# Kernel tuning notes

Measured on AMD Instinct MI355X. Metric: run time of the kernel, lower is better.

## Reference

```python
import jax, jax.numpy as jnp
import numpy as np

D_MODEL = 384
D_INNER = 768   # 2 * d_model
D_STATE = 16
DT_RANK = 24    # ceil(d_model/16)
K_CONV = 4
BATCH = 8
SEQ = 2048
EPS = 1e-5


def _layer_norm(x, w, b):
    mu = x.mean(-1, keepdims=True)
    var = ((x - mu) ** 2).mean(-1, keepdims=True)
    return (x - mu) * jax.lax.rsqrt(var + EPS) * w + b


def _silu(x):
    return x * jax.nn.sigmoid(x)


def _mamba_mixer(x, in_proj, conv_w, conv_b, x_proj, dt_w, dt_b, A_log, Dp, out_proj):
    # x: (B, L, d_model)
    xz = x @ in_proj.T                      # (B, L, 2*d_inner)
    xs, z = jnp.split(xz, 2, axis=-1)       # each (B, L, d_inner)
    # causal depthwise conv1d (pad left k-1)
    xc = jnp.transpose(xs, (0, 2, 1))       # (B, d_inner, L)
    xc = jnp.pad(xc, ((0, 0), (0, 0), (K_CONV - 1, 0)))
    xc = jax.lax.conv_general_dilated(
        xc, conv_w, window_strides=(1,), padding='VALID',
        feature_group_count=D_INNER,
        dimension_numbers=('NCH', 'OIH', 'NCH'))
    xs = _silu(jnp.transpose(xc, (0, 2, 1)) + conv_b)   # (B, L, d_inner)
    # input-dependent SSM parameters
    x_dbl = xs @ x_proj.T                    # (B, L, dt_rank + 2*d_state)
    dt, Bm, Cm = jnp.split(x_dbl, [DT_RANK, DT_RANK + D_STATE], axis=-1)
    dt = jax.nn.softplus(dt @ dt_w.T + dt_b)  # (B, L, d_inner)
    A = -jnp.exp(A_log)                       # (d_inner, d_state)

    def step(h, inp):
        dt_t, B_t, C_t, x_t = inp             # (B,d), (B,N), (B,N), (B,d)
        h = jnp.exp(dt_t[:, :, None] * A) * h + (dt_t * x_t)[:, :, None] * B_t[:, None, :]
        y = jnp.einsum('bdn,bn->bd', h, C_t)
        return h, y

    h0 = jnp.zeros((xs.shape[0], D_INNER, D_STATE), xs.dtype)
    inps = (jnp.moveaxis(dt, 1, 0), jnp.moveaxis(Bm, 1, 0),
            jnp.moveaxis(Cm, 1, 0), jnp.moveaxis(xs, 1, 0))
    _, ys = jax.lax.scan(step, h0, inps)      # ys: (L, B, d_inner)
    y = jnp.moveaxis(ys, 0, 1) + xs * Dp      # skip term D*x
    y = y * _silu(z)                          # gated output
    return y @ out_proj.T                     # (B, L, d_model)


def setup_inputs() -> dict:
    key = jax.random.key(0)
    ks = jax.random.split(key, 10)
    s = 0.02
    A_init = jnp.broadcast_to(jnp.log(jnp.arange(1, D_STATE + 1, dtype=jnp.float32)),
                              (2, D_INNER, D_STATE))
    return {
        'x': jax.random.normal(ks[0], (BATCH, SEQ, D_MODEL), jnp.float32),
        'norm_w': jnp.ones((2, D_MODEL), jnp.float32),
        'norm_b': jnp.zeros((2, D_MODEL), jnp.float32),
        'in_proj': jax.random.normal(ks[1], (2, 2 * D_INNER, D_MODEL)) * s,
        'conv_w': jax.random.normal(ks[2], (2, D_INNER, 1, K_CONV)) * 0.2,
        'conv_b': jax.random.normal(ks[3], (2, D_INNER)) * s,
        'x_proj': jax.random.normal(ks[4], (2, DT_RANK + 2 * D_STATE, D_INNER)) * s,
        'dt_w': jax.random.normal(ks[5], (2, D_INNER, DT_RANK)) * s,
        'dt_b': jax.random.normal(ks[6], (2, D_INNER)) * 0.1 - 4.0,
        'A_log': A_init,
        'Dp': jnp.ones((2, D_INNER), jnp.float32),
        'out_proj': jax.random.normal(ks[7], (2, D_MODEL, D_INNER)) * s,
    }


def reference(x, norm_w, norm_b, in_proj, conv_w, conv_b, x_proj, dt_w, dt_b, A_log, Dp, out_proj):
    def blk(i, h):
        return h + _mamba_mixer(_layer_norm(h, norm_w[i], norm_b[i]),
                                in_proj[i], conv_w[i], conv_b[i], x_proj[i],
                                dt_w[i], dt_b[i], A_log[i], Dp[i], out_proj[i])
    h = blk(0, x)                    # forward-direction block
    h = jnp.flip(h, axis=-2)         # reverse sequence
    h = blk(1, h)                    # backward-direction block
    return jnp.flip(h, axis=-2)      # restore order
```

## Files before the change

kernel.cpp:

```cpp
#include <hip/hip_runtime.h>
#include <hip/hip_bf16.h>
#include <cstddef>

#define D_MODEL 384
#define D_INNER 768
#define D_STATE 16
#define DT_RANK 24
#define K_CONV  4
#define BATCH   8
#define SEQ     2048
#define BL      (BATCH * SEQ)
#define NCHUNK  64
#define LCHUNK  (SEQ / NCHUNK)
#define XDBL_LD 64
#define LOG2E   1.44269504088896f

typedef unsigned short ushort_t;
typedef __bf16 bf16x8 __attribute__((ext_vector_type(8)));
typedef float  f32x4  __attribute__((ext_vector_type(4)));
typedef unsigned short u16x8 __attribute__((ext_vector_type(8)));

#define GLOBAL_AS(p) ((const __attribute__((address_space(1))) void*)(p))
#define LDS_AS(p)    ((__attribute__((address_space(3))) void*)(p))

__device__ __forceinline__ ushort_t f32_to_bf16_rne(float v) {
    unsigned int u = __float_as_uint(v);
    return (ushort_t)((u + 0x7FFFu + ((u >> 16) & 1u)) >> 16);
}
__device__ __forceinline__ float bf16_to_f32(ushort_t u) {
    return __uint_as_float(((unsigned int)u) << 16);
}

#define N_INP  (2 * 1536 * D_MODEL)
#define N_OUTP (2 * D_MODEL * D_INNER)
#define N_XP   (2 * 64 * D_INNER)
#define N_CW   (2 * K_CONV * D_INNER)
#define N_AL   (2 * D_STATE * D_INNER)
#define N_DW   (2 * DT_RANK * D_INNER)
#define N_PREP (N_INP + N_OUTP + N_XP + N_CW + N_AL + N_DW)

__global__ __launch_bounds__(256) void prep_kernel(
    const float* __restrict__ in_proj, const float* __restrict__ out_proj,
    const float* __restrict__ x_proj, const float* __restrict__ conv_w,
    const float* __restrict__ A_log, const float* __restrict__ dt_w,
    ushort_t* __restrict__ wbf_in, ushort_t* __restrict__ wbf_out,
    ushort_t* __restrict__ xp_bf, float* __restrict__ cwt,
    float* __restrict__ alt, float* __restrict__ dwt)
{
    int i = blockIdx.x * 256 + threadIdx.x;
    if (i < N_INP) {
        wbf_in[i] = f32_to_bf16_rne(in_proj[i]);
        return;
    }
    i -= N_INP;
    if (i < N_OUTP) {
        wbf_out[i] = f32_to_bf16_rne(out_proj[i]);
        return;
    }
    i -= N_OUTP;
    if (i < N_XP) {
        int c   = i % D_INNER;
        int r   = (i / D_INNER) % 64;
        int dir = i / (64 * D_INNER);
        xp_bf[i] = (r < 56)
            ? f32_to_bf16_rne(x_proj[((size_t)dir * 56 + r) * D_INNER + c])
            : (ushort_t)0;
        return;
    }
    i -= N_XP;
    if (i < N_CW) {
        int c = i % D_INNER, k = (i / D_INNER) % K_CONV, dir = i / (K_CONV * D_INNER);
        cwt[i] = conv_w[((size_t)dir * D_INNER + c) * K_CONV + k];
        return;
    }
    i -= N_CW;
    if (i < N_AL) {
        int d = i % D_INNER, n = (i / D_INNER) % D_STATE, dir = i / (D_STATE * D_INNER);
        alt[i] = A_log[((size_t)dir * D_INNER + d) * D_STATE + n];
        return;
    }
    i -= N_AL;
    if (i < N_DW) {
        int d = i % D_INNER, r = (i / D_INNER) % DT_RANK, dir = i / (DT_RANK * D_INNER);
        dwt[i] = dt_w[((size_t)dir * D_INNER + d) * DT_RANK + r];
    }
}

__global__ __launch_bounds__(256) void check_A_kernel(
    const float* __restrict__ A_log, int* __restrict__ flags)
{
    __shared__ int ok[2];
    int tid = threadIdx.x;
    if (tid < 2) ok[tid] = 1;
    __syncthreads();
    for (int dir = 0; dir < 2; dir++) {
        bool good = true;
        for (int j = tid; j < D_INNER * D_STATE; j += 256) {
            int n = j % D_STATE;
            float v = __expf(A_log[(size_t)dir * D_INNER * D_STATE + j]);
            good = good && (fabsf(v - (float)(n + 1)) <= 1e-4f * (float)(n + 1));
        }
        if (!good) atomicAnd(&ok[dir], 0);
    }
    __syncthreads();
    if (tid < 2) flags[tid] = ok[tid];
}

__global__ __launch_bounds__(384) void ln_kernel(
    const float* __restrict__ in, const float* __restrict__ w,
    const float* __restrict__ b, ushort_t* __restrict__ out)
{
    int row = blockIdx.x;
    int tid = threadIdx.x;
    float v = in[(size_t)row * D_MODEL + tid];
    float s = v, sq = v * v;
    #pragma unroll
    for (int o = 32; o; o >>= 1) {
        s  += __shfl_down(s, o);
        sq += __shfl_down(sq, o);
    }
    __shared__ float ss[6], ssq[6];
    __shared__ float mb[2];
    int wid = tid >> 6;
    if ((tid & 63) == 0) { ss[wid] = s; ssq[wid] = sq; }
    __syncthreads();
    if (tid == 0) {
        float S = 0.f, Q = 0.f;
        #pragma unroll
        for (int k = 0; k < 6; k++) { S += ss[k]; Q += ssq[k]; }
        float mu  = S * (1.0f / D_MODEL);
        float var = Q * (1.0f / D_MODEL) - mu * mu;
        mb[0] = mu;
        mb[1] = rsqrtf(var + 1e-5f);
    }
    __syncthreads();
    float r = (v - mb[0]) * mb[1] * w[tid] + b[tid];
    out[(size_t)row * D_MODEL + tid] = f32_to_bf16_rne(r);
}

__global__ __launch_bounds__(256) void gemm_mfma_b16(
    const ushort_t* __restrict__ A, const ushort_t* __restrict__ W,
    ushort_t* __restrict__ C, int N, int K)
{
    __shared__ __bf16 As[128 * 32];
    __shared__ __bf16 Ws[128 * 32];
    int tid  = threadIdx.x;
    int bm = blockIdx.x, bn = blockIdx.y;
    int lane = tid & 63, wave = tid >> 6;
    int wr = wave >> 1, wc = wave & 1;
    int quad = lane >> 4, l16 = lane & 15;
    int ca = ((quad ^ ((l16 >> 1) & 3))) * 8;
    int cbg = ((tid & 3) ^ ((tid >> 3) & 3)) * 8;

    const ushort_t* Ag = A + (size_t)(bm * 128 + (tid >> 2)) * K + cbg;
    const ushort_t* Wg = W + (size_t)(bn * 128 + (tid >> 2)) * K + cbg;

    f32x4 acc[4][4] = {};

    for (int k0 = 0; k0 < K; k0 += 32) {
        __syncthreads();
        __builtin_amdgcn_global_load_lds(GLOBAL_AS(Ag + k0),
                                         LDS_AS(As + tid * 8), 16, 0, 0);
        __builtin_amdgcn_global_load_lds(GLOBAL_AS(Ag + (size_t)64 * K + k0),
                                         LDS_AS(As + 2048 + tid * 8), 16, 0, 0);
        __builtin_amdgcn_global_load_lds(GLOBAL_AS(Wg + k0),
                                         LDS_AS(Ws + tid * 8), 16, 0, 0);
        __builtin_amdgcn_global_load_lds(GLOBAL_AS(Wg + (size_t)64 * K + k0),
                                         LDS_AS(Ws + 2048 + tid * 8), 16, 0, 0);
        __syncthreads();

        bf16x8 af[4], wf[4];
        #pragma unroll
        for (int i = 0; i < 4; i++)
            af[i] = *(const bf16x8*)(As + (wr * 64 + i * 16 + l16) * 32 + ca);
        #pragma unroll
        for (int j = 0; j < 4; j++)
            wf[j] = *(const bf16x8*)(Ws + (wc * 64 + j * 16 + l16) * 32 + ca);
        #pragma unroll
        for (int i = 0; i < 4; i++)
            #pragma unroll
            for (int j = 0; j < 4; j++)
                acc[i][j] = __builtin_amdgcn_mfma_f32_16x16x32_bf16(
                    af[i], wf[j], acc[i][j], 0, 0, 0);
    }

    #pragma unroll
    for (int i = 0; i < 4; i++) {
        #pragma unroll
        for (int r = 0; r < 4; r++) {
            int row = bm * 128 + wr * 64 + i * 16 + quad * 4 + r;
            #pragma unroll
            for (int j = 0; j < 4; j++) {
                int col = bn * 128 + wc * 64 + j * 16 + l16;
                C[(size_t)row * N + col] = f32_to_bf16_rne(acc[i][j][r]);
            }
        }
    }
}

__global__ __launch_bounds__(256) void gemm_mfma_f32(
    const ushort_t* __restrict__ A, const ushort_t* __restrict__ W,
    const float* __restrict__ resid, float* __restrict__ C, int N, int K)
{
    __shared__ __bf16 As[128 * 32];
    __shared__ __bf16 Ws[128 * 32];
    int tid  = threadIdx.x;
    int bm = blockIdx.x, bn = blockIdx.y;
    int lane = tid & 63, wave = tid >> 6;
    int wr = wave >> 1, wc = wave & 1;
    int quad = lane >> 4, l16 = lane & 15;
    int ca = ((quad ^ ((l16 >> 1) & 3))) * 8;
    int cbg = ((tid & 3) ^ ((tid >> 3) & 3)) * 8;

    const ushort_t* Ag = A + (size_t)(bm * 128 + (tid >> 2)) * K + cbg;
    const ushort_t* Wg = W + (size_t)(bn * 128 + (tid >> 2)) * K + cbg;

    f32x4 acc[4][4] = {};

    for (int k0 = 0; k0 < K; k0 += 32) {
        __syncthreads();
        __builtin_amdgcn_global_load_lds(GLOBAL_AS(Ag + k0),
                                         LDS_AS(As + tid * 8), 16, 0, 0);
        __builtin_amdgcn_global_load_lds(GLOBAL_AS(Ag + (size_t)64 * K + k0),
                                         LDS_AS(As + 2048 + tid * 8), 16, 0, 0);
        __builtin_amdgcn_global_load_lds(GLOBAL_AS(Wg + k0),
                                         LDS_AS(Ws + tid * 8), 16, 0, 0);
        __builtin_amdgcn_global_load_lds(GLOBAL_AS(Wg + (size_t)64 * K + k0),
                                         LDS_AS(Ws + 2048 + tid * 8), 16, 0, 0);
        __syncthreads();

        bf16x8 af[4], wf[4];
        #pragma unroll
        for (int i = 0; i < 4; i++)
            af[i] = *(const bf16x8*)(As + (wr * 64 + i * 16 + l16) * 32 + ca);
        #pragma unroll
        for (int j = 0; j < 4; j++)
            wf[j] = *(const bf16x8*)(Ws + (wc * 64 + j * 16 + l16) * 32 + ca);
        #pragma unroll
        for (int i = 0; i < 4; i++)
            #pragma unroll
            for (int j = 0; j < 4; j++)
                acc[i][j] = __builtin_amdgcn_mfma_f32_16x16x32_bf16(
                    af[i], wf[j], acc[i][j], 0, 0, 0);
    }

    #pragma unroll
    for (int i = 0; i < 4; i++) {
        #pragma unroll
        for (int r = 0; r < 4; r++) {
            int row = bm * 128 + wr * 64 + i * 16 + quad * 4 + r;
            #pragma unroll
            for (int j = 0; j < 4; j++) {
                int col = bn * 128 + wc * 64 + j * 16 + l16;
                size_t idx = (size_t)row * N + col;
                C[idx] = acc[i][j][r] + resid[idx];
            }
        }
    }
}

__global__ __launch_bounds__(256) void xdbl_mfma(
    const ushort_t* __restrict__ A, const ushort_t* __restrict__ W,
    float* __restrict__ C)
{
    __shared__ __bf16 As[128 * 32];
    __shared__ __bf16 Ws[64 * 32];
    int tid  = threadIdx.x;
    int bm = blockIdx.x;
    int lane = tid & 63, wave = tid >> 6;
    int quad = lane >> 4, l16 = lane & 15;
    int ca = ((quad ^ ((l16 >> 1) & 3))) * 8;
    int cbg = ((tid & 3) ^ ((tid >> 3) & 3)) * 8;

    const ushort_t* Ag = A + (size_t)(bm * 128 + (tid >> 2)) * D_INNER + cbg;
    const ushort_t* Wg = W + (size_t)(tid >> 2) * D_INNER + cbg;

    f32x4 acc[2][4] = {};

    for (int k0 = 0; k0 < D_INNER; k0 += 32) {
        __syncthreads();
        __builtin_amdgcn_global_load_lds(GLOBAL_AS(Ag + k0),
                                         LDS_AS(As + tid * 8), 16, 0, 0);
        __builtin_amdgcn_global_load_lds(GLOBAL_AS(Ag + (size_t)64 * D_INNER + k0),
                                         LDS_AS(As + 2048 + tid * 8), 16, 0, 0);
        __builtin_amdgcn_global_load_lds(GLOBAL_AS(Wg + k0),
                                         LDS_AS(Ws + tid * 8), 16, 0, 0);
        __syncthreads();

        bf16x8 af[2], wf[4];
        #pragma unroll
        for (int i = 0; i < 2; i++)
            af[i] = *(const bf16x8*)(As + (wave * 32 + i * 16 + l16) * 32 + ca);
        #pragma unroll
        for (int j = 0; j < 4; j++)
            wf[j] = *(const bf16x8*)(Ws + (j * 16 + l16) * 32 + ca);
        #pragma unroll
        for (int i = 0; i < 2; i++)
            #pragma unroll
            for (int j = 0; j < 4; j++)
                acc[i][j] = __builtin_amdgcn_mfma_f32_16x16x32_bf16(
                    af[i], wf[j], acc[i][j], 0, 0, 0);
    }

    #pragma unroll
    for (int i = 0; i < 2; i++) {
        #pragma unroll
        for (int r = 0; r < 4; r++) {
            int row = bm * 128 + wave * 32 + i * 16 + quad * 4 + r;
            #pragma unroll
            for (int j = 0; j < 4; j++) {
                int col = j * 16 + l16;
                C[(size_t)row * XDBL_LD + col] = acc[i][j][r];
            }
        }
    }
}

__global__ __launch_bounds__(256) void dt_kernel(
    const float* __restrict__ xdbl, const float* __restrict__ dwt,
    const float* __restrict__ dtbias, ushort_t* __restrict__ dtb)
{
    int g    = blockIdx.x % 3;
    int row0 = (blockIdx.x / 3) * 64;
    int tid  = threadIdx.x;
    int d    = g * 256 + tid;
    float w[DT_RANK];
    #pragma unroll
    for (int r = 0; r < DT_RANK; r++) w[r] = dwt[r * D_INNER + d];
    float bias = dtbias[d];
    __shared__ float xd[64][DT_RANK];
    for (int idx = tid; idx < 64 * DT_RANK; idx += 256) {
        int rr = idx / DT_RANK, cc = idx % DT_RANK;
        xd[rr][cc] = xdbl[(size_t)(row0 + rr) * XDBL_LD + cc];
    }
    __syncthreads();
    #pragma unroll 4
    for (int i = 0; i < 64; i++) {
        float acc = bias;
        #pragma unroll
        for (int r = 0; r < DT_RANK; r++) acc = fmaf(xd[i][r], w[r], acc);
        float sp = acc > 20.f ? acc : __logf(1.f + __expf(acc));
        dtb[(size_t)(row0 + i) * D_INNER + d] = f32_to_bf16_rne(sp);
    }
}

__global__ __launch_bounds__(256) void conv_silu_kernel(
    const ushort_t* __restrict__ xz, const float* __restrict__ cwt,
    const float* __restrict__ cb, ushort_t* __restrict__ xsc, int dir)
{
    int idx8 = blockIdx.x * 256 + threadIdx.x;
    int c8   = (idx8 % 96) * 8;
    int row  = idx8 / 96;
    int l    = row % SEQ;
    int b0   = row - l;

    float acc[8];
    float4 bv0 = *(const float4*)(cb + c8);
    float4 bv1 = *(const float4*)(cb + c8 + 4);
    acc[0] = bv0.x; acc[1] = bv0.y; acc[2] = bv0.z; acc[3] = bv0.w;
    acc[4] = bv1.x; acc[5] = bv1.y; acc[6] = bv1.z; acc[7] = bv1.w;

    #pragma unroll
    for (int k = 0; k < 4; k++) {
        int ls = dir ? (l + k) : (l - 3 + k);
        int wk = dir ? (3 - k) : k;
        bool ok = dir ? (ls < SEQ) : (ls >= 0);
        if (ok) {
            u16x8 v = *(const u16x8*)(xz + (size_t)(b0 + ls) * 1536 + c8);
            float4 w0 = *(const float4*)(cwt + wk * D_INNER + c8);
            float4 w1 = *(const float4*)(cwt + wk * D_INNER + c8 + 4);
            float wv[8] = {w0.x, w0.y, w0.z, w0.w, w1.x, w1.y, w1.z, w1.w};
            #pragma unroll
            for (int j = 0; j < 8; j++)
                acc[j] = fmaf(bf16_to_f32(v[j]), wv[j], acc[j]);
        }
    }
    u16x8 o;
    #pragma unroll
    for (int j = 0; j < 8; j++) {
        float sg = 1.0f / (1.0f + __expf(-acc[j]));
        o[j] = f32_to_bf16_rne(acc[j] * sg);
    }
    *(u16x8*)(xsc + (size_t)row * D_INNER + c8) = o;
}

#define SLOW_H(idx, bq) { \
    float a_ = *(const volatile float*)(alt + (idx) * D_INNER + d); \
    float e_ = __builtin_amdgcn_exp2f(dtv * (-__expf(a_) * LOG2E)); \
    h[idx] = fmaf(e_, h[idx], dtx * (bq)); }

template<int DIR>
__global__ __launch_bounds__(256, 8) void scan_pass1(
    const ushort_t* __restrict__ xsc, const ushort_t* __restrict__ dtb,
    const float* __restrict__ xdbl, const float* __restrict__ alt,
    const int* __restrict__ flag,
    ushort_t* __restrict__ hstate, float* __restrict__ sumdt_buf)
{
    int g = blockIdx.x % 3;
    int c = (blockIdx.x / 3) % NCHUNK;
    int b = blockIdx.x / (3 * NCHUNK);
    int d = g * 256 + threadIdx.x;
    float h[D_STATE] = {};
    float sdt = 0.f;

    const int l0 = DIR ? (SEQ - 1 - c * LCHUNK) : (c * LCHUNK);
    constexpr ptrdiff_t sN = DIR ? -(ptrdiff_t)D_INNER : (ptrdiff_t)D_INNER;
    constexpr ptrdiff_t sX = DIR ? -(ptrdiff_t)XDBL_LD : (ptrdiff_t)XDBL_LD;
    size_t row0 = (size_t)b * SEQ + l0;
    const ushort_t* pdt = dtb + row0 * D_INNER + d;
    const ushort_t* pxs = xsc + row0 * D_INNER + d;
    const float*    pbc = xdbl + row0 * XDBL_LD + DT_RANK;

    if (flag[0]) {
        #pragma unroll 2
        for (int i = 0; i < LCHUNK; i++) {
            float dtv = bf16_to_f32(*pdt);
            float xv  = bf16_to_f32(*pxs);
            float dtx = dtv * xv;
            sdt += dtv;
            float w1 = __builtin_amdgcn_exp2f(-dtv * LOG2E);
            float w2 = w1 * w1, w3 = w2 * w1, w4 = w2 * w2;
            float w8 = w4 * w4, w12 = w8 * w4;
            {
                float4 Bq = *(const float4*)(pbc);
                h[0] = fmaf(w1, h[0], dtx * Bq.x);
                h[1] = fmaf(w2, h[1], dtx * Bq.y);
                h[2] = fmaf(w3, h[2], dtx * Bq.z);
                h[3] = fmaf(w4, h[3], dtx * Bq.w);
            }
            {
                float4 Bq = *(const float4*)(pbc + 4);
                h[4] = fmaf(w4 * w1, h[4], dtx * Bq.x);
                h[5] = fmaf(w4 * w2, h[5], dtx * Bq.y);
                h[6] = fmaf(w4 * w3, h[6], dtx * Bq.z);
                h[7] = fmaf(w8,      h[7], dtx * Bq.w);
            }
            {
                float4 Bq = *(const float4*)(pbc + 8);
                h[8]  = fmaf(w8 * w1, h[8],  dtx * Bq.x);
                h[9]  = fmaf(w8 * w2, h[9],  dtx * Bq.y);
                h[10] = fmaf(w8 * w3, h[10], dtx * Bq.z);
                h[11] = fmaf(w12,     h[11], dtx * Bq.w);
            }
            {
                float4 Bq = *(const float4*)(pbc + 12);
                h[12] = fmaf(w12 * w1, h[12], dtx * Bq.x);
                h[13] = fmaf(w12 * w2, h[13], dtx * Bq.y);
                h[14] = fmaf(w12 * w3, h[14], dtx * Bq.z);
                h[15] = fmaf(w8 * w8,  h[15], dtx * Bq.w);
            }
            pdt += sN; pxs += sN; pbc += sX;
        }
    } else {
        for (int i = 0; i < LCHUNK; i++) {
            float dtv = bf16_to_f32(*pdt);
            float xv  = bf16_to_f32(*pxs);
            float dtx = dtv * xv;
            sdt += dtv;
            #pragma unroll
            for (int q = 0; q < 4; q++) {
                float4 Bq = *(const float4*)(pbc + 4 * q);
                SLOW_H(4*q+0, Bq.x); SLOW_H(4*q+1, Bq.y);
                SLOW_H(4*q+2, Bq.z); SLOW_H(4*q+3, Bq.w);
            }
            pdt += sN; pxs += sN; pbc += sX;
        }
    }
    size_t cidx = (size_t)(b * NCHUNK + c) * D_INNER + d;
    sumdt_buf[cidx] = sdt;
    #pragma unroll
    for (int n = 0; n < D_STATE; n++)
        hstate[cidx * D_STATE + n] = f32_to_bf16_rne(h[n]);
}

__global__ __launch_bounds__(256) void scan_pass2(
    ushort_t* __restrict__ hstate, const float* __restrict__ sumdt_buf,
    const float* __restrict__ alt)
{
    int gid = blockIdx.x * 256 + threadIdx.x;
    int n = gid & 15;
    int d = (gid >> 4) % D_INNER;
    int b = gid / (16 * D_INNER);
    float A2 = -__expf(alt[n * D_INNER + d]) * LOG2E;
    float h = 0.f;
    for (int c = 0; c < NCHUNK; c++) {
        size_t cidx = (size_t)(b * NCHUNK + c) * D_INNER + d;
        float ho = bf16_to_f32(hstate[cidx * D_STATE + n]);
        hstate[cidx * D_STATE + n] = f32_to_bf16_rne(h);
        h = fmaf(__builtin_amdgcn_exp2f(A2 * sumdt_buf[cidx]), h, ho);
    }
}

template<int DIR>
__global__ __launch_bounds__(256, 8) void scan_pass3(
    const ushort_t* __restrict__ xsc, const ushort_t* __restrict__ dtb,
    const ushort_t* __restrict__ xz, const float* __restrict__ xdbl,
    const float* __restrict__ alt, const float* __restrict__ Dp,
    const int* __restrict__ flag, const ushort_t* __restrict__ hstate,
    ushort_t* __restrict__ y)
{
    int g = blockIdx.x % 3;
    int c = (blockIdx.x / 3) % NCHUNK;
    int b = blockIdx.x / (3 * NCHUNK);
    int d = g * 256 + threadIdx.x;
    size_t cidx = (size_t)(b * NCHUNK + c) * D_INNER + d;
    float h[D_STATE];
    #pragma unroll
    for (int n = 0; n < D_STATE; n++)
        h[n] = bf16_to_f32(hstate[cidx * D_STATE + n]);
    float Dd = Dp[d];

    const int l0 = DIR ? (SEQ - 1 - c * LCHUNK) : (c * LCHUNK);
    constexpr ptrdiff_t sN = DIR ? -(ptrdiff_t)D_INNER : (ptrdiff_t)D_INNER;
    constexpr ptrdiff_t sX = DIR ? -(ptrdiff_t)XDBL_LD : (ptrdiff_t)XDBL_LD;
    constexpr ptrdiff_t sZ = DIR ? -(ptrdiff_t)1536 : (ptrdiff_t)1536;
    size_t row0 = (size_t)b * SEQ + l0;
    const ushort_t* pdt = dtb + row0 * D_INNER + d;
    const ushort_t* pxs = xsc + row0 * D_INNER + d;
    const ushort_t* pz  = xz  + row0 * 1536 + D_INNER + d;
    const float*    pbc = xdbl + row0 * XDBL_LD + DT_RANK;
    ushort_t*       py  = y + row0 * D_INNER + d;

    if (flag[0]) {
        for (int i = 0; i < LCHUNK; i++) {
            float dtv = bf16_to_f32(*pdt);
            float xv  = bf16_to_f32(*pxs);
            float zv  = bf16_to_f32(*pz);
            float dtx = dtv * xv;
            float w1 = __builtin_amdgcn_exp2f(-dtv * LOG2E);
            float w2 = w1 * w1, w3 = w2 * w1, w4 = w2 * w2;
            float w8 = w4 * w4, w12 = w8 * w4;
            float yv0 = 0.f, yv1 = 0.f;
            {
                float4 Bq = *(const float4*)(pbc);
                float4 Cq = *(const float4*)(pbc + D_STATE);
                h[0] = fmaf(w1, h[0], dtx * Bq.x);
                h[1] = fmaf(w2, h[1], dtx * Bq.y);
                h[2] = fmaf(w3, h[2], dtx * Bq.z);
                h[3] = fmaf(w4, h[3], dtx * Bq.w);
                yv0 = fmaf(h[0], Cq.x, yv0);
                yv1 = fmaf(h[1], Cq.y, yv1);
                yv0 = fmaf(h[2], Cq.z, yv0);
                yv1 = fmaf(h[3], Cq.w, yv1);
            }
            {
                float4 Bq = *(const float4*)(pbc + 4);
                float4 Cq = *(const float4*)(pbc + D_STATE + 4);
                h[4] = fmaf(w4 * w1, h[4], dtx * Bq.x);
                h[5] = fmaf(w4 * w2, h[5], dtx * Bq.y);
                h[6] = fmaf(w4 * w3, h[6], dtx * Bq.z);
                h[7] = fmaf(w8,      h[7], dtx * Bq.w);
                yv0 = fmaf(h[4], Cq.x, yv0);
                yv1 = fmaf(h[5], Cq.y, yv1);
                yv0 = fmaf(h[6], Cq.z, yv0);
                yv1 = fmaf(h[7], Cq.w, yv1);
            }
            {
                float4 Bq = *(const float4*)(pbc + 8);
                float4 Cq = *(const float4*)(pbc + D_STATE + 8);
                h[8]  = fmaf(w8 * w1, h[8],  dtx * Bq.x);
                h[9]  = fmaf(w8 * w2, h[9],  dtx * Bq.y);
                h[10] = fmaf(w8 * w3, h[10], dtx * Bq.z);
                h[11] = fmaf(w12,     h[11], dtx * Bq.w);
                yv0 = fmaf(h[8],  Cq.x, yv0);
                yv1 = fmaf(h[9],  Cq.y, yv1);
                yv0 = fmaf(h[10], Cq.z, yv0);
                yv1 = fmaf(h[11], Cq.w, yv1);
            }
            {
                float4 Bq = *(const float4*)(pbc + 12);
                float4 Cq = *(const float4*)(pbc + D_STATE + 12);
                h[12] = fmaf(w12 * w1, h[12], dtx * Bq.x);
                h[13] = fmaf(w12 * w2, h[13], dtx * Bq.y);
                h[14] = fmaf(w12 * w3, h[14], dtx * Bq.z);
                h[15] = fmaf(w8 * w8,  h[15], dtx * Bq.w);
                yv0 = fmaf(h[12], Cq.x, yv0);
                yv1 = fmaf(h[13], Cq.y, yv1);
                yv0 = fmaf(h[14], Cq.z, yv0);
                yv1 = fmaf(h[15], Cq.w, yv1);
            }
            float yv = fmaf(xv, Dd, yv0 + yv1);
            float sg = 1.f / (1.f + __expf(-zv));
            yv *= zv * sg;
            *py = f32_to_bf16_rne(yv);
            pdt += sN; pxs += sN; pz += sZ; pbc += sX; py += sN;
        }
    } else {
        for (int i = 0; i < LCHUNK; i++) {
            float dtv = bf16_to_f32(*pdt);
            float xv  = bf16_to_f32(*pxs);
            float zv  = bf16_to_f32(*pz);
            float dtx = dtv * xv;
            float yv0 = 0.f, yv1 = 0.f;
            #pragma unroll
            for (int q = 0; q < 4; q++) {
                float4 Bq = *(const float4*)(pbc + 4 * q);
                float4 Cq = *(const float4*)(pbc + D_STATE + 4 * q);
                SLOW_H(4*q+0, Bq.x); SLOW_H(4*q+1, Bq.y);
                SLOW_H(4*q+2, Bq.z); SLOW_H(4*q+3, Bq.w);
                yv0 = fmaf(h[4*q+0], Cq.x, yv0);
                yv1 = fmaf(h[4*q+1], Cq.y, yv1);
                yv0 = fmaf(h[4*q+2], Cq.z, yv0);
                yv1 = fmaf(h[4*q+3], Cq.w, yv1);
            }
            float yv = fmaf(xv, Dd, yv0 + yv1);
            float sg = 1.f / (1.f + __expf(-zv));
            yv *= zv * sg;
            *py = f32_to_bf16_rne(yv);
            pdt += sN; pxs += sN; pz += sZ; pbc += sX; py += sN;
        }
    }
}

extern "C" void kernel_launch(void* const* d_in, const int* in_sizes, int n_in,
                              void* d_out, int out_size, void* d_ws, size_t ws_size,
                              hipStream_t stream)
{
    const float* x       = (const float*)d_in[0];
    const float* norm_w  = (const float*)d_in[1];
    const float* norm_b  = (const float*)d_in[2];
    const float* in_proj = (const float*)d_in[3];
    const float* conv_w  = (const float*)d_in[4];
    const float* conv_b  = (const float*)d_in[5];
    const float* x_proj  = (const float*)d_in[6];
    const float* dt_w    = (const float*)d_in[7];
    const float* dt_b    = (const float*)d_in[8];
    const float* A_log   = (const float*)d_in[9];
    const float* Dp      = (const float*)d_in[10];
    const float* out_proj= (const float*)d_in[11];
    float* out = (float*)d_out;

    float* ws   = (float*)d_ws;
    float* reg0 = ws;                ws += (size_t)BL * D_INNER / 2;
    ushort_t* lnb = (ushort_t*)reg0;
    ushort_t* ybf = (ushort_t*)reg0;
    ushort_t* xzb  = (ushort_t*)ws;  ws += (size_t)BL * 1536 / 2;
    ushort_t* xscb = (ushort_t*)ws;  ws += (size_t)BL * D_INNER / 2;
    ushort_t* dtb  = (ushort_t*)ws;  ws += (size_t)BL * D_INNER / 2;
    float* xdbl = ws;                ws += (size_t)BL * XDBL_LD;
    float* sumdt  = ws;              ws += (size_t)BATCH * NCHUNK * D_INNER;
    ushort_t* hstate = (ushort_t*)ws; ws += (size_t)BATCH * NCHUNK * D_INNER * D_STATE / 2;
    ushort_t* wbf_in  = (ushort_t*)ws;  ws += (size_t)N_INP / 2;
    ushort_t* wbf_out = (ushort_t*)ws;  ws += (size_t)N_OUTP / 2;
    ushort_t* xp_bf   = (ushort_t*)ws;  ws += (size_t)N_XP / 2;
    float* cwt = ws;                 ws += (size_t)N_CW;
    float* alt = ws;                 ws += (size_t)N_AL;
    float* dwt = ws;                 ws += (size_t)N_DW;
    int* aflags = (int*)ws;          ws += 2;

    prep_kernel<<<N_PREP / 256, 256, 0, stream>>>(
        in_proj, out_proj, x_proj, conv_w, A_log, dt_w,
        wbf_in, wbf_out, xp_bf, cwt, alt, dwt);
    check_A_kernel<<<1, 256, 0, stream>>>(A_log, aflags);

    for (int i = 0; i < 2; i++) {
        const float* hinp = (i == 0) ? x : out;
        ln_kernel<<<BL, 384, 0, stream>>>(hinp, norm_w + i * D_MODEL,
                                          norm_b + i * D_MODEL, lnb);
        gemm_mfma_b16<<<dim3(BL / 128, 1536 / 128), 256, 0, stream>>>(
            lnb, wbf_in + (size_t)i * 1536 * D_MODEL, xzb, 1536, D_MODEL);
        conv_silu_kernel<<<(BL * 96) / 256, 256, 0, stream>>>(
            xzb, cwt + (size_t)i * K_CONV * D_INNER, conv_b + i * D_INNER,
            xscb, i);
        xdbl_mfma<<<BL / 128, 256, 0, stream>>>(
            xscb, xp_bf + (size_t)i * 64 * D_INNER, xdbl);
        dt_kernel<<<(BL / 64) * 3, 256, 0, stream>>>(
            xdbl, dwt + (size_t)i * DT_RANK * D_INNER, dt_b + i * D_INNER, dtb);
        if (i == 0) {
            scan_pass1<0><<<BATCH * NCHUNK * 3, 256, 0, stream>>>(
                xscb, dtb, xdbl, alt, aflags, hstate, sumdt);
        } else {
            scan_pass1<1><<<BATCH * NCHUNK * 3, 256, 0, stream>>>(
                xscb, dtb, xdbl, alt + (size_t)D_STATE * D_INNER,
                aflags + 1, hstate, sumdt);
        }
        scan_pass2<<<(BATCH * D_INNER * D_STATE) / 256, 256, 0, stream>>>(
            hstate, sumdt, alt + (size_t)i * D_STATE * D_INNER);
        if (i == 0) {
            scan_pass3<0><<<BATCH * NCHUNK * 3, 256, 0, stream>>>(
                xscb, dtb, xzb, xdbl, alt, Dp, aflags, hstate, ybf);
        } else {
            scan_pass3<1><<<BATCH * NCHUNK * 3, 256, 0, stream>>>(
                xscb, dtb, xzb, xdbl, alt + (size_t)D_STATE * D_INNER,
                Dp + D_INNER, aflags + 1, hstate, ybf);
        }
        gemm_mfma_f32<<<dim3(BL / 128, D_MODEL / 128), 256, 0, stream>>>(
            ybf, wbf_out + (size_t)i * D_MODEL * D_INNER, hinp, out,
            D_MODEL, D_INNER);
    }
}
```

Measured before the change: 495.3 us.

## Split scan state across thread pairs and stage B/C chunk in LDS

The scan pass1 and pass3 kernels now give each channel's 16 states to two threads of 8 states each, so the grid doubles and per-thread register pressure drops. The chunk's B and C vectors are loaded once per block into shared memory instead of every thread reading them from global memory each step. In pass3 the partial y sums are combined with a lane shuffle and only the even lane writes the output. Each dt/x/z element is now read twice, once by each lane of the pair, and the write predication leaves half the lanes idle for the epilogue.

```diff
diff --git a/kernel.cpp b/kernel.cpp
--- a/kernel.cpp
+++ b/kernel.cpp
@@ -384,10 +384,10 @@
     *(u16x8*)(xsc + (size_t)row * D_INNER + c8) = o;
 }
 
-#define SLOW_H(idx, bq) { \
-    float a_ = *(const volatile float*)(alt + (idx) * D_INNER + d); \
+#define SLOW_H2(n, bq) { \
+    float a_ = *(const volatile float*)(alt + (s8 + (n)) * D_INNER + d); \
     float e_ = __builtin_amdgcn_exp2f(dtv * (-__expf(a_) * LOG2E)); \
-    h[idx] = fmaf(e_, h[idx], dtx * (bq)); }
+    h[n] = fmaf(e_, h[n], dtx * (bq)); }
 
 template<int DIR>
 __global__ __launch_bounds__(256, 8) void scan_pass1(
@@ -396,20 +396,32 @@
     const int* __restrict__ flag,
     ushort_t* __restrict__ hstate, float* __restrict__ sumdt_buf)
 {
-    int g = blockIdx.x % 3;
-    int c = (blockIdx.x / 3) % NCHUNK;
-    int b = blockIdx.x / (3 * NCHUNK);
-    int d = g * 256 + threadIdx.x;
-    float h[D_STATE] = {};
+    int g = blockIdx.x % 6;
+    int c = (blockIdx.x / 6) % NCHUNK;
+    int b = blockIdx.x / (6 * NCHUNK);
+    int tid = threadIdx.x;
+    int s   = tid & 1;
+    int s8  = s * 8;
+    int d   = g * 128 + (tid >> 1);
+
+    const int l0 = DIR ? (SEQ - 1 - c * LCHUNK) : (c * LCHUNK);
+    size_t row0 = (size_t)b * SEQ + l0;
+
+    __shared__ float sBC[LCHUNK][32];
+    {
+        int i  = tid >> 3;
+        int cc = (tid & 7) * 4;
+        size_t rg = row0 + (DIR ? -(ptrdiff_t)i : (ptrdiff_t)i);
+        *(float4*)&sBC[i][cc] =
+            *(const float4*)(xdbl + rg * XDBL_LD + DT_RANK + cc);
+    }
+    __syncthreads();
+
+    float h[8] = {};
     float sdt = 0.f;
-
-    const int l0 = DIR ? (SEQ - 1 - c * LCHUNK) : (c * LCHUNK);
     constexpr ptrdiff_t sN = DIR ? -(ptrdiff_t)D_INNER : (ptrdiff_t)D_INNER;
-    constexpr ptrdiff_t sX = DIR ? -(ptrdiff_t)XDBL_LD : (ptrdiff_t)XDBL_LD;
-    size_t row0 = (size_t)b * SEQ + l0;
     const ushort_t* pdt = dtb + row0 * D_INNER + d;
     const ushort_t* pxs = xsc + row0 * D_INNER + d;
-    const float*    pbc = xdbl + row0 * XDBL_LD + DT_RANK;
 
     if (flag[0]) {
         #pragma unroll 2
@@ -419,37 +431,21 @@
             float dtx = dtv * xv;
             sdt += dtv;
             float w1 = __builtin_amdgcn_exp2f(-dtv * LOG2E);
-            float w2 = w1 * w1, w3 = w2 * w1, w4 = w2 * w2;
-            float w8 = w4 * w4, w12 = w8 * w4;
-            {
-                float4 Bq = *(const float4*)(pbc);
-                h[0] = fmaf(w1, h[0], dtx * Bq.x);
-                h[1] = fmaf(w2, h[1], dtx * Bq.y);
-                h[2] = fmaf(w3, h[2], dtx * Bq.z);
-                h[3] = fmaf(w4, h[3], dtx * Bq.w);
-            }
-            {
-                float4 Bq = *(const float4*)(pbc + 4);
-                h[4] = fmaf(w4 * w1, h[4], dtx * Bq.x);
-                h[5] = fmaf(w4 * w2, h[5], dtx * Bq.y);
-                h[6] = fmaf(w4 * w3, h[6], dtx * Bq.z);
-                h[7] = fmaf(w8,      h[7], dtx * Bq.w);
-            }
-            {
-                float4 Bq = *(const float4*)(pbc + 8);
-                h[8]  = fmaf(w8 * w1, h[8],  dtx * Bq.x);
-                h[9]  = fmaf(w8 * w2, h[9],  dtx * Bq.y);
-                h[10] = fmaf(w8 * w3, h[10], dtx * Bq.z);
-                h[11] = fmaf(w12,     h[11], dtx * Bq.w);
-            }
-            {
-                float4 Bq = *(const float4*)(pbc + 12);
-                h[12] = fmaf(w12 * w1, h[12], dtx * Bq.x);
-                h[13] = fmaf(w12 * w2, h[13], dtx * Bq.y);
-                h[14] = fmaf(w12 * w3, h[14], dtx * Bq.z);
-                h[15] = fmaf(w8 * w8,  h[15], dtx * Bq.w);
-            }
-            pdt += sN; pxs += sN; pbc += sX;
+            float w2 = w1 * w1, w3 = w2 * w1, w4 = w2 * w2, w8 = w4 * w4;
+            float m  = s ? w8 : 1.0f;
+            float f1 = m * w1, f2 = m * w2, f3 = m * w3, f4 = m * w4;
+            float f5 = f4 * w1, f6 = f4 * w2, f7 = f4 * w3, f8 = m * w8;
+            float4 B0 = *(const float4*)&sBC[i][s8];
+            float4 B1 = *(const float4*)&sBC[i][s8 + 4];
+            h[0] = fmaf(f1, h[0], dtx * B0.x);
+            h[1] = fmaf(f2, h[1], dtx * B0.y);
+            h[2] = fmaf(f3, h[2], dtx * B0.z);
+            h[3] = fmaf(f4, h[3], dtx * B0.w);
+            h[4] = fmaf(f5, h[4], dtx * B1.x);
+            h[5] = fmaf(f6, h[5], dtx * B1.y);
+            h[6] = fmaf(f7, h[6], dtx * B1.z);
+            h[7] = fmaf(f8, h[7], dtx * B1.w);
+            pdt += sN; pxs += sN;
         }
     } else {
         for (int i = 0; i < LCHUNK; i++) {
@@ -457,20 +453,21 @@
             float xv  = bf16_to_f32(*pxs);
             float dtx = dtv * xv;
             sdt += dtv;
-            #pragma unroll
-            for (int q = 0; q < 4; q++) {
-                float4 Bq = *(const float4*)(pbc + 4 * q);
-                SLOW_H(4*q+0, Bq.x); SLOW_H(4*q+1, Bq.y);
-                SLOW_H(4*q+2, Bq.z); SLOW_H(4*q+3, Bq.w);
-            }
-            pdt += sN; pxs += sN; pbc += sX;
+            float4 B0 = *(const float4*)&sBC[i][s8];
+            float4 B1 = *(const float4*)&sBC[i][s8 + 4];
+            SLOW_H2(0, B0.x); SLOW_H2(1, B0.y);
+            SLOW_H2(2, B0.z); SLOW_H2(3, B0.w);
+            SLOW_H2(4, B1.x); SLOW_H2(5, B1.y);
+            SLOW_H2(6, B1.z); SLOW_H2(7, B1.w);
+            pdt += sN; pxs += sN;
         }
     }
     size_t cidx = (size_t)(b * NCHUNK + c) * D_INNER + d;
-    sumdt_buf[cidx] = sdt;
-    #pragma unroll
-    for (int n = 0; n < D_STATE; n++)
-        hstate[cidx * D_STATE + n] = f32_to_bf16_rne(h[n]);
+    if (!s) sumdt_buf[cidx] = sdt;
+    u16x8 hv;
+    #pragma unroll
+    for (int n = 0; n < 8; n++) hv[n] = f32_to_bf16_rne(h[n]);
+    *(u16x8*)(hstate + cidx * D_STATE + s8) = hv;
 }
 
 __global__ __launch_bounds__(256) void scan_pass2(
@@ -499,91 +496,85 @@
     const int* __restrict__ flag, const ushort_t* __restrict__ hstate,
     ushort_t* __restrict__ y)
 {
-    int g = blockIdx.x % 3;
-    int c = (blockIdx.x / 3) % NCHUNK;
-    int b = blockIdx.x / (3 * NCHUNK);
-    int d = g * 256 + threadIdx.x;
+    int g = blockIdx.x % 6;
+    int c = (blockIdx.x / 6) % NCHUNK;
+    int b = blockIdx.x / (6 * NCHUNK);
+    int tid = threadIdx.x;
+    int s   = tid & 1;
+    int s8  = s * 8;
+    int d   = g * 128 + (tid >> 1);
+
+    const int l0 = DIR ? (SEQ - 1 - c * LCHUNK) : (c * LCHUNK);
+    size_t row0 = (size_t)b * SEQ + l0;
+
+    __shared__ float sBC[LCHUNK][32];
+    {
+        int i  = tid >> 3;
+        int cc = (tid & 7) * 4;
+        size_t rg = row0 + (DIR ? -(ptrdiff_t)i : (ptrdiff_t)i);
+        *(float4*)&sBC[i][cc] =
+            *(const float4*)(xdbl + rg * XDBL_LD + DT_RANK + cc);
+    }
+    __syncthreads();
+
     size_t cidx = (size_t)(b * NCHUNK + c) * D_INNER + d;
-    float h[D_STATE];
-    #pragma unroll
-    for (int n = 0; n < D_STATE; n++)
-        h[n] = bf16_to_f32(hstate[cidx * D_STATE + n]);
+    float h[8];
+    {
+        u16x8 hv = *(const u16x8*)(hstate + cidx * D_STATE + s8);
+        #pragma unroll
+        for (int n = 0; n < 8; n++) h[n] = bf16_to_f32(hv[n]);
+    }
     float Dd = Dp[d];
 
-    const int l0 = DIR ? (SEQ - 1 - c * LCHUNK) : (c * LCHUNK);
     constexpr ptrdiff_t sN = DIR ? -(ptrdiff_t)D_INNER : (ptrdiff_t)D_INNER;
-    constexpr ptrdiff_t sX = DIR ? -(ptrdiff_t)XDBL_LD : (ptrdiff_t)XDBL_LD;
     constexpr ptrdiff_t sZ = DIR ? -(ptrdiff_t)1536 : (ptrdiff_t)1536;
-    size_t row0 = (size_t)b * SEQ + l0;
     const ushort_t* pdt = dtb + row0 * D_INNER + d;
     const ushort_t* pxs = xsc + row0 * D_INNER + d;
     const ushort_t* pz  = xz  + row0 * 1536 + D_INNER + d;
-    const float*    pbc = xdbl + row0 * XDBL_LD + DT_RANK;
     ushort_t*       py  = y + row0 * D_INNER + d;
 
     if (flag[0]) {
+        #pragma unroll 2
         for (int i = 0; i < LCHUNK; i++) {
             float dtv = bf16_to_f32(*pdt);
             float xv  = bf16_to_f32(*pxs);
             float zv  = bf16_to_f32(*pz);
             float dtx = dtv * xv;
             float w1 = __builtin_amdgcn_exp2f(-dtv * LOG2E);
-            float w2 = w1 * w1, w3 = w2 * w1, w4 = w2 * w2;
-            float w8 = w4 * w4, w12 = w8 * w4;
+            float w2 = w1 * w1, w3 = w2 * w1, w4 = w2 * w2, w8 = w4 * w4;
+            float m  = s ? w8 : 1.0f;
+            float f1 = m * w1, f2 = m * w2, f3 = m * w3, f4 = m * w4;
+            float f5 = f4 * w1, f6 = f4 * w2, f7 = f4 * w3, f8 = m * w8;
+            float4 B0 = *(const float4*)&sBC[i][s8];
+            float4 B1 = *(const float4*)&sBC[i][s8 + 4];
+            float4 C0 = *(const float4*)&sBC[i][16 + s8];
+            float4 C1 = *(const float4*)&sBC[i][16 + s8 + 4];
             float yv0 = 0.f, yv1 = 0.f;
-            {
-                float4 Bq = *(const float4*)(pbc);
-                float4 Cq = *(const float4*)(pbc + D_STATE);
-                h[0] = fmaf(w1, h[0], dtx * Bq.x);
-                h[1] = fmaf(w2, h[1], dtx * Bq.y);
-                h[2] = fmaf(w3, h[2], dtx * Bq.z);
-                h[3] = fmaf(w4, h[3], dtx * Bq.w);
-                yv0 = fmaf(h[0], Cq.x, yv0);
-                yv1 = fmaf(h[1], Cq.y, yv1);
-                yv0 = fmaf(h[2], Cq.z, yv0);
-                yv1 = fmaf(h[3], Cq.w, yv1);
+            h[0] = fmaf(f1, h[0], dtx * B0.x);
+            h[1] = fmaf(f2, h[1], dtx * B0.y);
+            h[2] = fmaf(f3, h[2], dtx * B0.z);
+            h[3] = fmaf(f4, h[3], dtx * B0.w);
+            yv0 = fmaf(h[0], C0.x, yv0);
+            yv1 = fmaf(h[1], C0.y, yv1);
+            yv0 = fmaf(h[2], C0.z, yv0);
+            yv1 = fmaf(h[3], C0.w, yv1);
+            h[4] = fmaf(f5, h[4], dtx * B1.x);
+            h[5] = fmaf(f6, h[5], dtx * B1.y);
+            h[6] = fmaf(f7, h[6], dtx * B1.z);
+            h[7] = fmaf(f8, h[7], dtx * B1.w);
+            yv0 = fmaf(h[4], C1.x, yv0);
+            yv1 = fmaf(h[5], C1.y, yv1);
+            yv0 = fmaf(h[6], C1.z, yv0);
+            yv1 = fmaf(h[7], C1.w, yv1);
+            float yp = yv0 + yv1;
+            float yo = yp + __shfl_xor(yp, 1);
+            if (!s) {
+                float yv = fmaf(xv, Dd, yo);
+                float sg = 1.f / (1.f + __expf(-zv));
+                yv *= zv * sg;
+                *py = f32_to_bf16_rne(yv);
             }
-            {
-                float4 Bq = *(const float4*)(pbc + 4);
-                float4 Cq = *(const float4*)(pbc + D_STATE + 4);
-                h[4] = fmaf(w4 * w1, h[4], dtx * Bq.x);
-                h[5] = fmaf(w4 * w2, h[5], dtx * Bq.y);
-                h[6] = fmaf(w4 * w3, h[6], dtx * Bq.z);
-                h[7] = fmaf(w8,      h[7], dtx * Bq.w);
-                yv0 = fmaf(h[4], Cq.x, yv0);
-                yv1 = fmaf(h[5], Cq.y, yv1);
-                yv0 = fmaf(h[6], Cq.z, yv0);
-                yv1 = fmaf(h[7], Cq.w, yv1);
-            }
-            {
-                float4 Bq = *(const float4*)(pbc + 8);
-                float4 Cq = *(const float4*)(pbc + D_STATE + 8);
-                h[8]  = fmaf(w8 * w1, h[8],  dtx * Bq.x);
-                h[9]  = fmaf(w8 * w2, h[9],  dtx * Bq.y);
-                h[10] = fmaf(w8 * w3, h[10], dtx * Bq.z);
-                h[11] = fmaf(w12,     h[11], dtx * Bq.w);
-                yv0 = fmaf(h[8],  Cq.x, yv0);
-                yv1 = fmaf(h[9],  Cq.y, yv1);
-                yv0 = fmaf(h[10], Cq.z, yv0);
-                yv1 = fmaf(h[11], Cq.w, yv1);
-            }
-            {
-                float4 Bq = *(const float4*)(pbc + 12);
-                float4 Cq = *(const float4*)(pbc + D_STATE + 12);
-                h[12] = fmaf(w12 * w1, h[12], dtx * Bq.x);
-                h[13] = fmaf(w12 * w2, h[13], dtx * Bq.y);
-                h[14] = fmaf(w12 * w3, h[14], dtx * Bq.z);
-                h[15] = fmaf(w8 * w8,  h[15], dtx * Bq.w);
-                yv0 = fmaf(h[12], Cq.x, yv0);
-                yv1 = fmaf(h[13], Cq.y, yv1);
-                yv0 = fmaf(h[14], Cq.z, yv0);
-                yv1 = fmaf(h[15], Cq.w, yv1);
-            }
-            float yv = fmaf(xv, Dd, yv0 + yv1);
-            float sg = 1.f / (1.f + __expf(-zv));
-            yv *= zv * sg;
-            *py = f32_to_bf16_rne(yv);
-            pdt += sN; pxs += sN; pz += sZ; pbc += sX; py += sN;
+            pdt += sN; pxs += sN; pz += sZ; py += sN;
         }
     } else {
         for (int i = 0; i < LCHUNK; i++) {
@@ -591,23 +582,32 @@
             float xv  = bf16_to_f32(*pxs);
             float zv  = bf16_to_f32(*pz);
             float dtx = dtv * xv;
+            float4 B0 = *(const float4*)&sBC[i][s8];
+            float4 B1 = *(const float4*)&sBC[i][s8 + 4];
+            float4 C0 = *(const float4*)&sBC[i][16 + s8];
+            float4 C1 = *(const float4*)&sBC[i][16 + s8 + 4];
             float yv0 = 0.f, yv1 = 0.f;
-            #pragma unroll
-            for (int q = 0; q < 4; q++) {
-                float4 Bq = *(const float4*)(pbc + 4 * q);
-                float4 Cq = *(const float4*)(pbc + D_STATE + 4 * q);
-                SLOW_H(4*q+0, Bq.x); SLOW_H(4*q+1, Bq.y);
-                SLOW_H(4*q+2, Bq.z); SLOW_H(4*q+3, Bq.w);
-                yv0 = fmaf(h[4*q+0], Cq.x, yv0);
-                yv1 = fmaf(h[4*q+1], Cq.y, yv1);
-                yv0 = fmaf(h[4*q+2], Cq.z, yv0);
-                yv1 = fmaf(h[4*q+3], Cq.w, yv1);
+            SLOW_H2(0, B0.x); SLOW_H2(1, B0.y);
+            SLOW_H2(2, B0.z); SLOW_H2(3, B0.w);
+            yv0 = fmaf(h[0], C0.x, yv0);
+            yv1 = fmaf(h[1], C0.y, yv1);
+            yv0 = fmaf(h[2], C0.z, yv0);
+            yv1 = fmaf(h[3], C0.w, yv1);
+            SLOW_H2(4, B1.x); SLOW_H2(5, B1.y);
+            SLOW_H2(6, B1.z); SLOW_H2(7, B1.w);
+            yv0 = fmaf(h[4], C1.x, yv0);
+            yv1 = fmaf(h[5], C1.y, yv1);
+            yv0 = fmaf(h[6], C1.z, yv0);
+            yv1 = fmaf(h[7], C1.w, yv1);
+            float yp = yv0 + yv1;
+            float yo = yp + __shfl_xor(yp, 1);
+            if (!s) {
+                float yv = fmaf(xv, Dd, yo);
+                float sg = 1.f / (1.f + __expf(-zv));
+                yv *= zv * sg;
+                *py = f32_to_bf16_rne(yv);
             }
-            float yv = fmaf(xv, Dd, yv0 + yv1);
-            float sg = 1.f / (1.f + __expf(-zv));
-            yv *= zv * sg;
-            *py = f32_to_bf16_rne(yv);
-            pdt += sN; pxs += sN; pz += sZ; pbc += sX; py += sN;
+            pdt += sN; pxs += sN; pz += sZ; py += sN;
         }
     }
 }
@@ -667,20 +667,20 @@
         dt_kernel<<<(BL / 64) * 3, 256, 0, stream>>>(
             xdbl, dwt + (size_t)i * DT_RANK * D_INNER, dt_b + i * D_INNER, dtb);
         if (i == 0) {
-            scan_pass1<0><<<BATCH * NCHUNK * 3, 256, 0, stream>>>(
+            scan_pass1<0><<<BATCH * NCHUNK * 6, 256, 0, stream>>>(
                 xscb, dtb, xdbl, alt, aflags, hstate, sumdt);
         } else {
-            scan_pass1<1><<<BATCH * NCHUNK * 3, 256, 0, stream>>>(
+            scan_pass1<1><<<BATCH * NCHUNK * 6, 256, 0, stream>>>(
                 xscb, dtb, xdbl, alt + (size_t)D_STATE * D_INNER,
                 aflags + 1, hstate, sumdt);
         }
         scan_pass2<<<(BATCH * D_INNER * D_STATE) / 256, 256, 0, stream>>>(
             hstate, sumdt, alt + (size_t)i * D_STATE * D_INNER);
         if (i == 0) {
-            scan_pass3<0><<<BATCH * NCHUNK * 3, 256, 0, stream>>>(
+            scan_pass3<0><<<BATCH * NCHUNK * 6, 256, 0, stream>>>(
                 xscb, dtb, xzb, xdbl, alt, Dp, aflags, hstate, ybf);
         } else {
-            scan_pass3<1><<<BATCH * NCHUNK * 3, 256, 0, stream>>>(
+            scan_pass3<1><<<BATCH * NCHUNK * 6, 256, 0, stream>>>(
                 xscb, dtb, xzb, xdbl, alt + (size_t)D_STATE * D_INNER,
                 Dp + D_INNER, aflags + 1, hstate, ybf);
         }
```

New measurement: 545.6 us. +10.2%, slower.
